# Optimization experiments

Measured on AMD Instinct MI355X. Metric: run time of the kernel, lower is better.

Reference implementation:

```python
import jax, jax.numpy as jnp
import numpy as np

N = 100000
E = 1600000
F_IN = 512
HID = 8
HEADS = 8
NCLS = 16
NEG_SLOPE = 0.2
EPS = 1e-16


def gat_conv(x, W, att_src, att_dst, bias, src, dst, heads, ch, concat):
    n = x.shape[0]
    xl = (x @ W).reshape(n, heads, ch)              # [N,H,C]
    a_src = (xl * att_src).sum(-1)                  # [N,H]
    a_dst = (xl * att_dst).sum(-1)                  # [N,H]
    alpha = jax.nn.leaky_relu(a_src[src] + a_dst[dst], NEG_SLOPE)  # [E,H]
    amax = jax.ops.segment_max(alpha, dst, num_segments=n)         # [N,H]
    ex = jnp.exp(alpha - amax[dst])                                 # [E,H]
    denom = jax.ops.segment_sum(ex, dst, num_segments=n)           # [N,H]
    coef = ex / (denom[dst] + EPS)                                  # [E,H]
    msg = xl[src] * coef[:, :, None]                                # [E,H,C]
    out = jax.ops.segment_sum(msg, dst, num_segments=n)            # [N,H,C]
    out = out.reshape(n, heads * ch) if concat else out.mean(axis=1)
    return out + bias


def setup_inputs() -> dict:
    key = jax.random.key(0)
    ks = jax.random.split(key, 12)
    x = jax.random.normal(ks[0], (N, F_IN), dtype=jnp.float32)
    edge_index = jax.random.randint(ks[1], (2, E), 0, N, dtype=jnp.int32)
    s1 = 1.0 / np.sqrt(F_IN)
    s2 = 1.0 / np.sqrt(HID * HEADS)
    return {
        "x": x,
        "edge_index": edge_index,
        "W1": jax.random.normal(ks[2], (F_IN, HEADS * HID), dtype=jnp.float32) * s1,
        "att_src1": jax.random.normal(ks[3], (HEADS, HID), dtype=jnp.float32),
        "att_dst1": jax.random.normal(ks[4], (HEADS, HID), dtype=jnp.float32),
        "bias1": jnp.zeros((HEADS * HID,), dtype=jnp.float32),
        "W2": jax.random.normal(ks[5], (HEADS * HID, NCLS), dtype=jnp.float32) * s2,
        "att_src2": jax.random.normal(ks[6], (1, NCLS), dtype=jnp.float32),
        "att_dst2": jax.random.normal(ks[7], (1, NCLS), dtype=jnp.float32),
        "bias2": jnp.zeros((NCLS,), dtype=jnp.float32),
    }


def reference(x, edge_index, W1, att_src1, att_dst1, bias1, W2, att_src2, att_dst2, bias2):
    src, dst = edge_index[0], edge_index[1]
    # eval mode: all dropout layers are identity
    h = gat_conv(x, W1, att_src1, att_dst1, bias1, src, dst, HEADS, HID, True)
    h = jax.nn.elu(h)
    out = gat_conv(h, W2, att_src2, att_dst2, bias2, src, dst, 1, NCLS, False)
    return out
```

## Files before the change

### kernel.cpp

```cpp
#include <hip/hip_runtime.h>
#include <math.h>

#define N_NODES 100000
#define N_EDGES 1600000
#define F_IN    512
#define HID     8
#define HEADS   8
#define NCLS    16
#define NEG_SLOPE 0.2f
#define EPS_F   1e-16f
#define DEG_CAP 64
#define G1_BLOCKS 782
#define CSR_EPB 1024
#define CSR_BLOCKS 1563

__device__ __forceinline__ float lrelu(float a) {
    return a >= 0.f ? a : NEG_SLOPE * a;
}
__device__ __forceinline__ unsigned short f2bf_rne(float f) {
    unsigned b = __float_as_uint(f);
    b += 0x7FFFu + ((b >> 16) & 1u);
    return (unsigned short)(b >> 16);
}
__device__ __forceinline__ float bf2f(unsigned short u) {
    return __uint_as_float(((unsigned)u) << 16);
}

__global__ __launch_bounds__(256) void fused1_kernel(
    const float* __restrict__ x, const float* __restrict__ W1,
    const float* __restrict__ att_src, const float* __restrict__ att_dst,
    unsigned short* __restrict__ xl1b,
    float* __restrict__ a_src1, float* __restrict__ a_dst1,
    const int* __restrict__ src, const int* __restrict__ dst,
    int* __restrict__ cnt, int* __restrict__ csr_src) {
    __shared__ float xs[128][33];
    __shared__ float wsh[32][68];
    const int tid = threadIdx.x;

    if (blockIdx.x >= G1_BLOCKS) {
        int e0 = (blockIdx.x - G1_BLOCKS) * CSR_EPB + tid;
        int d[4], s[4];
        bool v[4];
#pragma unroll
        for (int q = 0; q < 4; q++) {
            int e = e0 + q * 256;
            v[q] = e < N_EDGES;
            if (v[q]) { d[q] = dst[e]; s[q] = src[e]; }
        }
        int pos[4];
#pragma unroll
        for (int q = 0; q < 4; q++)
            if (v[q]) pos[q] = atomicAdd(&cnt[d[q]], 1);
#pragma unroll
        for (int q = 0; q < 4; q++)
            if (v[q] && pos[q] < DEG_CAP)
                csr_src[(size_t)d[q] * DEG_CAP + pos[q]] = s[q];
        return;
    }

    const int nb  = blockIdx.x * 128;
    const int ng  = tid >> 3;
    const int cg  = tid & 7;

    float acc[4][8];
#pragma unroll
    for (int i = 0; i < 4; i++)
#pragma unroll
        for (int j = 0; j < 8; j++) acc[i][j] = 0.f;

    for (int kb = 0; kb < F_IN; kb += 32) {
#pragma unroll
        for (int q = 0; q < 4; q++) {
            int idx = tid + q * 256;
            int nl  = idx >> 3;
            int kq  = (idx & 7) * 4;
            int node = nb + nl; if (node >= N_NODES) node = N_NODES - 1;
            float4 vv = *(const float4*)&x[(size_t)node * F_IN + kb + kq];
            xs[nl][kq + 0] = vv.x; xs[nl][kq + 1] = vv.y;
            xs[nl][kq + 2] = vv.z; xs[nl][kq + 3] = vv.w;
        }
#pragma unroll
        for (int q = 0; q < 2; q++) {
            int idx = tid + q * 256;
            int kk  = idx >> 4;
            int cq  = (idx & 15) * 4;
            *(float4*)&wsh[kk][cq] = *(const float4*)&W1[(size_t)(kb + kk) * 64 + cq];
        }
        __syncthreads();
#pragma unroll
        for (int kk = 0; kk < 32; kk++) {
            float xa0 = xs[ng * 4 + 0][kk];
            float xa1 = xs[ng * 4 + 1][kk];
            float xa2 = xs[ng * 4 + 2][kk];
            float xa3 = xs[ng * 4 + 3][kk];
            float4 w0 = *(const float4*)&wsh[kk][cg * 8];
            float4 w1 = *(const float4*)&wsh[kk][cg * 8 + 4];
            float wa[8] = {w0.x, w0.y, w0.z, w0.w, w1.x, w1.y, w1.z, w1.w};
#pragma unroll
            for (int j = 0; j < 8; j++) {
                acc[0][j] += xa0 * wa[j];
                acc[1][j] += xa1 * wa[j];
                acc[2][j] += xa2 * wa[j];
                acc[3][j] += xa3 * wa[j];
            }
        }
        __syncthreads();
    }
    float4 s0 = *(const float4*)&att_src[cg * 8];
    float4 s1 = *(const float4*)&att_src[cg * 8 + 4];
    float4 d0 = *(const float4*)&att_dst[cg * 8];
    float4 d1 = *(const float4*)&att_dst[cg * 8 + 4];
    float sv[8] = {s0.x, s0.y, s0.z, s0.w, s1.x, s1.y, s1.z, s1.w};
    float dv[8] = {d0.x, d0.y, d0.z, d0.w, d1.x, d1.y, d1.z, d1.w};
#pragma unroll
    for (int i = 0; i < 4; i++) {
        int node = nb + ng * 4 + i;
        if (node < N_NODES) {
            unsigned pk[4];
#pragma unroll
            for (int j = 0; j < 4; j++)
                pk[j] = (unsigned)f2bf_rne(acc[i][2 * j]) |
                        ((unsigned)f2bf_rne(acc[i][2 * j + 1]) << 16);
            *(uint4*)&xl1b[(size_t)node * 64 + cg * 8] =
                make_uint4(pk[0], pk[1], pk[2], pk[3]);
            float as = 0.f, ad = 0.f;
#pragma unroll
            for (int j = 0; j < 8; j++) { as += acc[i][j] * sv[j]; ad += acc[i][j] * dv[j]; }
            a_src1[node * 8 + cg] = as;
            a_dst1[node * 8 + cg] = ad;
        }
    }
}

__global__ __launch_bounds__(256) void aggr1_kernel(
    const int* __restrict__ cnt, const int* __restrict__ csr_src,
    const float* __restrict__ a_src1, const float* __restrict__ a_dst1,
    const unsigned short* __restrict__ xl1b,
    const float* __restrict__ bias1, const float* __restrict__ W2,
    const float* __restrict__ att_src2, const float* __restrict__ att_dst2,
    char* __restrict__ pk2, float* __restrict__ a_dst2) {
    __shared__ float w2s[64][17];
    __shared__ float b1s[64];
    __shared__ float hbuf[8][64];
    const int tid  = threadIdx.x;
    const int w    = tid >> 6;
    const int lane = tid & 63;
    const int l32  = lane & 31;
    const int hf   = lane >> 5;
    const int c0   = l32 * 2;
    const int h    = l32 >> 2;

#pragma unroll
    for (int q = 0; q < 4; q++) {
        int idx = tid * 4 + q;
        w2s[idx >> 4][idx & 15] = W2[idx];
    }
    if (tid < 64) b1s[tid] = bias1[tid];
    __syncthreads();

    const int nl = w * 2 + hf;
    const int n  = blockIdx.x * 8 + nl;
    const int* bucket = &csr_src[(size_t)n * DEG_CAP];
    int c = cnt[n]; c = c < DEG_CAP ? c : DEG_CAP;
    int cw = c; { int co = __shfl_xor(c, 32); cw = cw > co ? cw : co; }
    float ad = a_dst1[n * 8 + h];
    float l = 0.f, acc0 = 0.f, acc1 = 0.f;

    for (int i = 0; i < cw; i += 8) {
        int s[8]; float e[8], x0[8], x1[8];
#pragma unroll
        for (int q = 0; q < 8; q++) {
            int ii = i + q; ii = ii < c ? ii : (c > 0 ? c - 1 : 0);
            s[q] = bucket[ii];
        }
#pragma unroll
        for (int q = 0; q < 8; q++) {
            int ss = s[q]; ss = ss < 0 ? 0 : ss;
            s[q] = ss >= N_NODES ? N_NODES - 1 : ss;
        }
#pragma unroll
        for (int q = 0; q < 8; q++) {
            unsigned v = *(const unsigned*)&xl1b[(size_t)s[q] * 64 + c0];
            x0[q] = bf2f((unsigned short)(v & 0xFFFFu));
            x1[q] = bf2f((unsigned short)(v >> 16));
        }
#pragma unroll
        for (int q = 0; q < 8; q++) {
            float al = lrelu(a_src1[s[q] * 8 + h] + ad);
            float ee = __expf(al);
            e[q] = (i + q < c) ? ee : 0.f;
        }
#pragma unroll
        for (int q = 0; q < 8; q++) {
            l += e[q]; acc0 += e[q] * x0[q]; acc1 += e[q] * x1[q];
        }
    }

    float dinv = 1.f / (l + EPS_F);
    float h0 = acc0 * dinv + b1s[c0];
    float h1 = acc1 * dinv + b1s[c0 + 1];
    h0 = h0 > 0.f ? h0 : (__expf(h0) - 1.f);
    h1 = h1 > 0.f ? h1 : (__expf(h1) - 1.f);
    hbuf[nl][c0] = h0; hbuf[nl][c0 + 1] = h1;
    __syncthreads();

    const int j  = l32 & 15;
    const int kh = l32 >> 4;
    float p = 0.f;
#pragma unroll
    for (int k2 = 0; k2 < 32; k2++) {
        int k = kh * 32 + k2;
        p += hbuf[nl][k] * w2s[k][j];
    }
    p += __shfl_xor(p, 16);
    float ss = p * att_src2[j];
    float dd = p * att_dst2[j];
#pragma unroll
    for (int mm = 8; mm >= 1; mm >>= 1) {
        ss += __shfl_xor(ss, mm);
        dd += __shfl_xor(dd, mm);
    }
    char* prow = pk2 + (size_t)n * 64;
    if (l32 < 16) ((unsigned short*)prow)[l32] = f2bf_rne(p);
    if (l32 == 0) {
        *(float*)(prow + 32) = ss;
        a_dst2[n] = dd;
    }
}

__global__ __launch_bounds__(256) void aggr2_kernel(
    const int* __restrict__ cnt, const int* __restrict__ csr_src,
    const char* __restrict__ pk2, const float* __restrict__ a_dst2,
    const float* __restrict__ bias2, float* __restrict__ out) {
    int idx = blockIdx.x * 256 + threadIdx.x;
    int n = idx >> 4;
    int j = idx & 15;
    if (n >= N_NODES) return;
    const int* bucket = &csr_src[(size_t)n * DEG_CAP];
    int c = cnt[n]; c = c < DEG_CAP ? c : DEG_CAP;
    int cw = c;
    { int co = __shfl_xor(c, 16); cw = cw > co ? cw : co; }
    { int co = __shfl_xor(cw, 32); cw = cw > co ? cw : co; }
    float ad = a_dst2[n];
    float l = 0.f, acc = 0.f;
    for (int i = 0; i < cw; i += 8) {
        int s[8]; float e[8], xv[8];
#pragma unroll
        for (int q = 0; q < 8; q++) {
            int ii = i + q; ii = ii < c ? ii : (c > 0 ? c - 1 : 0);
            s[q] = bucket[ii];
        }
#pragma unroll
        for (int q = 0; q < 8; q++) {
            int ssx = s[q]; ssx = ssx < 0 ? 0 : ssx;
            s[q] = ssx >= N_NODES ? N_NODES - 1 : ssx;
        }
#pragma unroll
        for (int q = 0; q < 8; q++) {
            const char* pr = pk2 + (size_t)s[q] * 64;
            xv[q] = bf2f(*(const unsigned short*)(pr + 2 * j));
        }
#pragma unroll
        for (int q = 0; q < 8; q++) {
            float as = *(const float*)(pk2 + (size_t)s[q] * 64 + 32);
            float al = lrelu(as + ad);
            float ee = __expf(al);
            e[q] = (i + q < c) ? ee : 0.f;
        }
#pragma unroll
        for (int q = 0; q < 8; q++) {
            l += e[q]; acc += e[q] * xv[q];
        }
    }
    out[(size_t)n * 16 + j] = acc / (l + EPS_F) + bias2[j];
}

extern "C" void kernel_launch(void* const* d_in, const int* in_sizes, int n_in,
                              void* d_out, int out_size, void* d_ws, size_t ws_size,
                              hipStream_t stream) {
    const float* x        = (const float*)d_in[0];
    const int*   ei       = (const int*)d_in[1];
    const float* W1       = (const float*)d_in[2];
    const float* att_src1 = (const float*)d_in[3];
    const float* att_dst1 = (const float*)d_in[4];
    const float* bias1    = (const float*)d_in[5];
    const float* W2       = (const float*)d_in[6];
    const float* att_src2 = (const float*)d_in[7];
    const float* att_dst2 = (const float*)d_in[8];
    const float* bias2    = (const float*)d_in[9];
    float* out = (float*)d_out;

    const int* src = ei;
    const int* dst = ei + N_EDGES;

    float* ws = (float*)d_ws;
    float* a_src1 = ws;
    float* a_dst1 = a_src1 + (size_t)N_NODES * 8;
    char*  pk2    = (char*)(a_dst1 + (size_t)N_NODES * 8);
    float* a_src2 = (float*)(pk2 + (size_t)N_NODES * 64);
    float* a_dst2 = a_src2 + N_NODES;
    int*   cnt    = (int*)(a_dst2 + N_NODES);
    int*   csr_src= cnt + N_NODES;
    unsigned short* xl1b = (unsigned short*)(csr_src + (size_t)N_NODES * DEG_CAP);

    hipMemsetAsync(cnt, 0, (size_t)N_NODES * sizeof(int), stream);

    fused1_kernel<<<G1_BLOCKS + CSR_BLOCKS, 256, 0, stream>>>(
        x, W1, att_src1, att_dst1, xl1b, a_src1, a_dst1,
        src, dst, cnt, csr_src);

    aggr1_kernel<<<N_NODES / 8, 256, 0, stream>>>(
        cnt, csr_src, a_src1, a_dst1, xl1b, bias1, W2, att_src2, att_dst2,
        pk2, a_dst2);

    aggr2_kernel<<<(N_NODES * 16 + 255) / 256, 256, 0, stream>>>(
        cnt, csr_src, pk2, a_dst2, bias2, out);
}
```

Measured before the change: 434.4 us.

## Fuse both aggregation kernels into one cooperative persistent kernel with grid sync

Result: slower. 702.2 us (+61.7%).

```diff
diff --git a/kernel.cpp b/kernel.cpp
--- a/kernel.cpp
+++ b/kernel.cpp
@@ -1,5 +1,8 @@
 #include <hip/hip_runtime.h>
+#include <hip/hip_cooperative_groups.h>
 #include <math.h>
+
+namespace cg = cooperative_groups;
 
 #define N_NODES 100000
 #define N_EDGES 1600000
@@ -13,6 +16,7 @@
 #define G1_BLOCKS 782
 #define CSR_EPB 1024
 #define CSR_BLOCKS 1563
+#define N_CUS 256
 
 __device__ __forceinline__ float lrelu(float a) {
     return a >= 0.f ? a : NEG_SLOPE * a;
@@ -132,6 +136,130 @@
     }
 }
 
+__device__ __forceinline__ void aggr1_body(
+    int n, int w_nl, int lane,
+    const int* __restrict__ cnt, const int* __restrict__ csr_src,
+    const float* __restrict__ a_src1, const float* __restrict__ a_dst1,
+    const unsigned short* __restrict__ xl1b,
+    const float (*w2s)[17], const float* b1s, float (*hbuf)[64],
+    const float* __restrict__ att_src2, const float* __restrict__ att_dst2,
+    char* __restrict__ pk2, float* __restrict__ a_dst2) {
+    const int l32  = lane & 31;
+    const int c0   = l32 * 2;
+    const int h    = l32 >> 2;
+
+    const int* bucket = &csr_src[(size_t)n * DEG_CAP];
+    int c = cnt[n]; c = c < DEG_CAP ? c : DEG_CAP;
+    int cw = c; { int co = __shfl_xor(c, 32); cw = cw > co ? cw : co; }
+    float ad = a_dst1[n * 8 + h];
+    float l = 0.f, acc0 = 0.f, acc1 = 0.f;
+
+    for (int i = 0; i < cw; i += 8) {
+        int s[8]; float e[8], x0[8], x1[8];
+#pragma unroll
+        for (int q = 0; q < 8; q++) {
+            int ii = i + q; ii = ii < c ? ii : (c > 0 ? c - 1 : 0);
+            s[q] = bucket[ii];
+        }
+#pragma unroll
+        for (int q = 0; q < 8; q++) {
+            int ss = s[q]; ss = ss < 0 ? 0 : ss;
+            s[q] = ss >= N_NODES ? N_NODES - 1 : ss;
+        }
+#pragma unroll
+        for (int q = 0; q < 8; q++) {
+            unsigned v = *(const unsigned*)&xl1b[(size_t)s[q] * 64 + c0];
+            x0[q] = bf2f((unsigned short)(v & 0xFFFFu));
+            x1[q] = bf2f((unsigned short)(v >> 16));
+        }
+#pragma unroll
+        for (int q = 0; q < 8; q++) {
+            float al = lrelu(a_src1[s[q] * 8 + h] + ad);
+            float ee = __expf(al);
+            e[q] = (i + q < c) ? ee : 0.f;
+        }
+#pragma unroll
+        for (int q = 0; q < 8; q++) {
+            l += e[q]; acc0 += e[q] * x0[q]; acc1 += e[q] * x1[q];
+        }
+    }
+
+    float dinv = 1.f / (l + EPS_F);
+    float h0 = acc0 * dinv + b1s[c0];
+    float h1 = acc1 * dinv + b1s[c0 + 1];
+    h0 = h0 > 0.f ? h0 : (__expf(h0) - 1.f);
+    h1 = h1 > 0.f ? h1 : (__expf(h1) - 1.f);
+    hbuf[w_nl][c0] = h0; hbuf[w_nl][c0 + 1] = h1;
+    __syncthreads();
+
+    const int j  = l32 & 15;
+    const int kh = l32 >> 4;
+    float p = 0.f;
+#pragma unroll
+    for (int k2 = 0; k2 < 32; k2++) {
+        int k = kh * 32 + k2;
+        p += hbuf[w_nl][k] * w2s[k][j];
+    }
+    p += __shfl_xor(p, 16);
+    float ss = p * att_src2[j];
+    float dd = p * att_dst2[j];
+#pragma unroll
+    for (int mm = 8; mm >= 1; mm >>= 1) {
+        ss += __shfl_xor(ss, mm);
+        dd += __shfl_xor(dd, mm);
+    }
+    char* prow = pk2 + (size_t)n * 64;
+    if (l32 < 16) ((unsigned short*)prow)[l32] = f2bf_rne(p);
+    if (l32 == 0) {
+        *(float*)(prow + 32) = ss;
+        a_dst2[n] = dd;
+    }
+}
+
+__device__ __forceinline__ void aggr2_body(
+    int n, int j,
+    const int* __restrict__ cnt, const int* __restrict__ csr_src,
+    const char* __restrict__ pk2, const float* __restrict__ a_dst2,
+    const float* __restrict__ bias2, float* __restrict__ out) {
+    const int* bucket = &csr_src[(size_t)n * DEG_CAP];
+    int c = cnt[n]; c = c < DEG_CAP ? c : DEG_CAP;
+    int cw = c;
+    { int co = __shfl_xor(c, 16); cw = cw > co ? cw : co; }
+    { int co = __shfl_xor(cw, 32); cw = cw > co ? cw : co; }
+    float ad = a_dst2[n];
+    float l = 0.f, acc = 0.f;
+    for (int i = 0; i < cw; i += 8) {
+        int s[8]; float e[8], xv[8];
+#pragma unroll
+        for (int q = 0; q < 8; q++) {
+            int ii = i + q; ii = ii < c ? ii : (c > 0 ? c - 1 : 0);
+            s[q] = bucket[ii];
+        }
+#pragma unroll
+        for (int q = 0; q < 8; q++) {
+            int ssx = s[q]; ssx = ssx < 0 ? 0 : ssx;
+            s[q] = ssx >= N_NODES ? N_NODES - 1 : ssx;
+        }
+#pragma unroll
+        for (int q = 0; q < 8; q++) {
+            const char* pr = pk2 + (size_t)s[q] * 64;
+            xv[q] = bf2f(*(const unsigned short*)(pr + 2 * j));
+        }
+#pragma unroll
+        for (int q = 0; q < 8; q++) {
+            float as = *(const float*)(pk2 + (size_t)s[q] * 64 + 32);
+            float al = lrelu(as + ad);
+            float ee = __expf(al);
+            e[q] = (i + q < c) ? ee : 0.f;
+        }
+#pragma unroll
+        for (int q = 0; q < 8; q++) {
+            l += e[q]; acc += e[q] * xv[q];
+        }
+    }
+    out[(size_t)n * 16 + j] = acc / (l + EPS_F) + bias2[j];
+}
+
 __global__ __launch_bounds__(256) void aggr1_kernel(
     const int* __restrict__ cnt, const int* __restrict__ csr_src,
     const float* __restrict__ a_src1, const float* __restrict__ a_dst1,
@@ -143,13 +271,6 @@
     __shared__ float b1s[64];
     __shared__ float hbuf[8][64];
     const int tid  = threadIdx.x;
-    const int w    = tid >> 6;
-    const int lane = tid & 63;
-    const int l32  = lane & 31;
-    const int hf   = lane >> 5;
-    const int c0   = l32 * 2;
-    const int h    = l32 >> 2;
-
 #pragma unroll
     for (int q = 0; q < 4; q++) {
         int idx = tid * 4 + q;
@@ -157,75 +278,12 @@
     }
     if (tid < 64) b1s[tid] = bias1[tid];
     __syncthreads();
-
-    const int nl = w * 2 + hf;
-    const int n  = blockIdx.x * 8 + nl;
-    const int* bucket = &csr_src[(size_t)n * DEG_CAP];
-    int c = cnt[n]; c = c < DEG_CAP ? c : DEG_CAP;
-    int cw = c; { int co = __shfl_xor(c, 32); cw = cw > co ? cw : co; }
-    float ad = a_dst1[n * 8 + h];
-    float l = 0.f, acc0 = 0.f, acc1 = 0.f;
-
-    for (int i = 0; i < cw; i += 8) {
-        int s[8]; float e[8], x0[8], x1[8];
-#pragma unroll
-        for (int q = 0; q < 8; q++) {
-            int ii = i + q; ii = ii < c ? ii : (c > 0 ? c - 1 : 0);
-            s[q] = bucket[ii];
-        }
-#pragma unroll
-        for (int q = 0; q < 8; q++) {
-            int ss = s[q]; ss = ss < 0 ? 0 : ss;
-            s[q] = ss >= N_NODES ? N_NODES - 1 : ss;
-        }
-#pragma unroll
-        for (int q = 0; q < 8; q++) {
-            unsigned v = *(const unsigned*)&xl1b[(size_t)s[q] * 64 + c0];
-            x0[q] = bf2f((unsigned short)(v & 0xFFFFu));
-            x1[q] = bf2f((unsigned short)(v >> 16));
-        }
-#pragma unroll
-        for (int q = 0; q < 8; q++) {
-            float al = lrelu(a_src1[s[q] * 8 + h] + ad);
-            float ee = __expf(al);
-            e[q] = (i + q < c) ? ee : 0.f;
-        }
-#pragma unroll
-        for (int q = 0; q < 8; q++) {
-            l += e[q]; acc0 += e[q] * x0[q]; acc1 += e[q] * x1[q];
-        }
-    }
-
-    float dinv = 1.f / (l + EPS_F);
-    float h0 = acc0 * dinv + b1s[c0];
-    float h1 = acc1 * dinv + b1s[c0 + 1];
-    h0 = h0 > 0.f ? h0 : (__expf(h0) - 1.f);
-    h1 = h1 > 0.f ? h1 : (__expf(h1) - 1.f);
-    hbuf[nl][c0] = h0; hbuf[nl][c0 + 1] = h1;
-    __syncthreads();
-
-    const int j  = l32 & 15;
-    const int kh = l32 >> 4;
-    float p = 0.f;
-#pragma unroll
-    for (int k2 = 0; k2 < 32; k2++) {
-        int k = kh * 32 + k2;
-        p += hbuf[nl][k] * w2s[k][j];
-    }
-    p += __shfl_xor(p, 16);
-    float ss = p * att_src2[j];
-    float dd = p * att_dst2[j];
-#pragma unroll
-    for (int mm = 8; mm >= 1; mm >>= 1) {
-        ss += __shfl_xor(ss, mm);
-        dd += __shfl_xor(dd, mm);
-    }
-    char* prow = pk2 + (size_t)n * 64;
-    if (l32 < 16) ((unsigned short*)prow)[l32] = f2bf_rne(p);
-    if (l32 == 0) {
-        *(float*)(prow + 32) = ss;
-        a_dst2[n] = dd;
-    }
+    const int w    = tid >> 6;
+    const int lane = tid & 63;
+    const int nl   = w * 2 + (lane >> 5);
+    const int n    = blockIdx.x * 8 + nl;
+    aggr1_body(n, nl, lane, cnt, csr_src, a_src1, a_dst1, xl1b,
+               w2s, b1s, hbuf, att_src2, att_dst2, pk2, a_dst2);
 }
 
 __global__ __launch_bounds__(256) void aggr2_kernel(
@@ -236,43 +294,47 @@
     int n = idx >> 4;
     int j = idx & 15;
     if (n >= N_NODES) return;
-    const int* bucket = &csr_src[(size_t)n * DEG_CAP];
-    int c = cnt[n]; c = c < DEG_CAP ? c : DEG_CAP;
-    int cw = c;
-    { int co = __shfl_xor(c, 16); cw = cw > co ? cw : co; }
-    { int co = __shfl_xor(cw, 32); cw = cw > co ? cw : co; }
-    float ad = a_dst2[n];
-    float l = 0.f, acc = 0.f;
-    for (int i = 0; i < cw; i += 8) {
-        int s[8]; float e[8], xv[8];
-#pragma unroll
-        for (int q = 0; q < 8; q++) {
-            int ii = i + q; ii = ii < c ? ii : (c > 0 ? c - 1 : 0);
-            s[q] = bucket[ii];
-        }
-#pragma unroll
-        for (int q = 0; q < 8; q++) {
-            int ssx = s[q]; ssx = ssx < 0 ? 0 : ssx;
-            s[q] = ssx >= N_NODES ? N_NODES - 1 : ssx;
-        }
-#pragma unroll
-        for (int q = 0; q < 8; q++) {
-            const char* pr = pk2 + (size_t)s[q] * 64;
-            xv[q] = bf2f(*(const unsigned short*)(pr + 2 * j));
-        }
-#pragma unroll
-        for (int q = 0; q < 8; q++) {
-            float as = *(const float*)(pk2 + (size_t)s[q] * 64 + 32);
-            float al = lrelu(as + ad);
-            float ee = __expf(al);
-            e[q] = (i + q < c) ? ee : 0.f;
-        }
-#pragma unroll
-        for (int q = 0; q < 8; q++) {
-            l += e[q]; acc += e[q] * xv[q];
-        }
-    }
-    out[(size_t)n * 16 + j] = acc / (l + EPS_F) + bias2[j];
+    aggr2_body(n, j, cnt, csr_src, pk2, a_dst2, bias2, out);
+}
+
+__global__ __launch_bounds__(256, 4) void aggr_fused_kernel(
+    const int* __restrict__ cnt, const int* __restrict__ csr_src,
+    const float* __restrict__ a_src1, const float* __restrict__ a_dst1,
+    const unsigned short* __restrict__ xl1b,
+    const float* __restrict__ bias1, const float* __restrict__ W2,
+    const float* __restrict__ att_src2, const float* __restrict__ att_dst2,
+    const float* __restrict__ bias2,
+    char* __restrict__ pk2, float* __restrict__ a_dst2,
+    float* __restrict__ out) {
+    __shared__ float w2s[64][17];
+    __shared__ float b1s[64];
+    __shared__ float hbuf[8][64];
+    const int tid  = threadIdx.x;
+#pragma unroll
+    for (int q = 0; q < 4; q++) {
+        int idx = tid * 4 + q;
+        w2s[idx >> 4][idx & 15] = W2[idx];
+    }
+    if (tid < 64) b1s[tid] = bias1[tid];
+    __syncthreads();
+    const int w    = tid >> 6;
+    const int lane = tid & 63;
+    const int nl   = w * 2 + (lane >> 5);
+
+    for (int u = blockIdx.x; u < N_NODES / 8; u += gridDim.x) {
+        aggr1_body(u * 8 + nl, nl, lane, cnt, csr_src, a_src1, a_dst1, xl1b,
+                   w2s, b1s, hbuf, att_src2, att_dst2, pk2, a_dst2);
+        __syncthreads();
+    }
+
+    __threadfence();
+    cg::this_grid().sync();
+    __threadfence();
+
+    for (int idx = blockIdx.x * 256 + tid; idx < N_NODES * 16;
+         idx += gridDim.x * 256) {
+        aggr2_body(idx >> 4, idx & 15, cnt, csr_src, pk2, a_dst2, bias2, out);
+    }
 }
 
 extern "C" void kernel_launch(void* const* d_in, const int* in_sizes, int n_in,
@@ -309,10 +371,28 @@
         x, W1, att_src1, att_dst1, xl1b, a_src1, a_dst1,
         src, dst, cnt, csr_src);
 
-    aggr1_kernel<<<N_NODES / 8, 256, 0, stream>>>(
-        cnt, csr_src, a_src1, a_dst1, xl1b, bias1, W2, att_src2, att_dst2,
-        pk2, a_dst2);
-
-    aggr2_kernel<<<(N_NODES * 16 + 255) / 256, 256, 0, stream>>>(
-        cnt, csr_src, pk2, a_dst2, bias2, out);
-}
+    int nb = 0;
+    hipError_t qe = hipOccupancyMaxActiveBlocksPerMultiprocessor(
+        &nb, (const void*)aggr_fused_kernel, 256, 0);
+    bool coop_ok = false;
+    if (qe == hipSuccess && nb > 0) {
+        int grid = nb * N_CUS;
+        if (grid > 2048) grid = 2048;
+        void* args[] = {
+            (void*)&cnt, (void*)&csr_src, (void*)&a_src1, (void*)&a_dst1,
+            (void*)&xl1b, (void*)&bias1, (void*)&W2, (void*)&att_src2,
+            (void*)&att_dst2, (void*)&bias2, (void*)&pk2, (void*)&a_dst2,
+            (void*)&out};
+        hipError_t ce = hipLaunchCooperativeKernel(
+            (const void*)aggr_fused_kernel, dim3(grid), dim3(256), args, 0,
+            stream);
+        coop_ok = (ce == hipSuccess);
+    }
+    if (!coop_ok) {
+        aggr1_kernel<<<N_NODES / 8, 256, 0, stream>>>(
+            cnt, csr_src, a_src1, a_dst1, xl1b, bias1, W2, att_src2, att_dst2,
+            pk2, a_dst2);
+        aggr2_kernel<<<(N_NODES * 16 + 255) / 256, 256, 0, stream>>>(
+            cnt, csr_src, pk2, a_dst2, bias2, out);
+    }
+}
```
